# Kernel tuning notes

Measured on AMD Instinct MI355X. Metric: run time of the kernel, lower is better.

## Reference

```python
import jax, jax.numpy as jnp
import numpy as np
import math

SEQ = 2048
N_EMBD = 2048
N_HEAD = 16
DIM = N_EMBD // N_HEAD  # 128


def setup_inputs() -> dict:
    key = jax.random.key(0)
    k1, k2, k3, k4, k5 = jax.random.split(key, 5)
    s = 1.0 / math.sqrt(N_EMBD)
    return {
        "hidden_states": jax.random.normal(k1, (SEQ, N_EMBD), dtype=jnp.float32),
        "Wqkv": jax.random.normal(k2, (N_HEAD, N_EMBD, 3 * DIM), dtype=jnp.float32) * s,
        "bqkv": jax.random.normal(k3, (N_HEAD, 3 * DIM), dtype=jnp.float32) * 0.02,
        "Wout": jax.random.normal(k4, (N_EMBD, N_EMBD), dtype=jnp.float32) * s,
        "bout": jax.random.normal(k5, (N_EMBD,), dtype=jnp.float32) * 0.02,
    }


def reference(hidden_states, Wqkv, bqkv, Wout, bout):
    # per-head qkv projection: [h, s, 3*dim]
    qkv = jnp.einsum("se,hed->hsd", hidden_states, Wqkv) + bqkv[:, None, :]
    q, k, v = qkv[..., :DIM], qkv[..., DIM:2 * DIM], qkv[..., 2 * DIM:]
    # NOTE: original divides by sqrt(n_embd), not sqrt(head_dim)
    scale = 1.0 / math.sqrt(N_EMBD)
    scores = jnp.einsum("hsd,htd->hst", q, k) * scale  # [h, s, s]
    causal = jnp.tril(jnp.ones((SEQ, SEQ), dtype=bool))
    scores = jnp.where(causal[None], scores, -jnp.inf)
    probs = jax.nn.softmax(scores, axis=-1)
    out = jnp.einsum("hst,htd->hsd", probs, v)  # [h, s, dim]
    out = jnp.transpose(out, (1, 0, 2)).reshape(SEQ, N_EMBD)  # concat heads
    return out @ Wout + bout
```

## Files before the change

### kernel.cpp

```cpp
#include <hip/hip_runtime.h>
#include <cfloat>

#define SEQ   2048
#define NE    2048
#define NH    16
#define DIM   128
#define NKV   384
#define QSCALE 0.022097086912079611f

typedef __attribute__((ext_vector_type(8))) short bf16x8;
typedef __attribute__((ext_vector_type(4))) float f32x4;
typedef __attribute__((ext_vector_type(16))) float f32x16;
typedef __attribute__((ext_vector_type(8))) unsigned short u16x8;
typedef __attribute__((ext_vector_type(4))) unsigned int u32x4;
typedef __attribute__((ext_vector_type(2))) unsigned int u32x2;

#define PSLOT_B 16896u
#define NUNITS  768

__device__ __forceinline__ unsigned short f32_to_bf16_rn(float x) {
    unsigned u = __builtin_bit_cast(unsigned, x);
    u += 0x7fffu + ((u >> 16) & 1u);
    return (unsigned short)(u >> 16);
}

__device__ __forceinline__ unsigned cvt_pk_bf16(float lo, float hi) {
    unsigned r;
    asm("v_cvt_pk_bf16_f32 %0, %1, %2" : "=v"(r) : "v"(lo), "v"(hi));
    return r;
}
__device__ __forceinline__ float bf16lo(unsigned w) {
    return __builtin_bit_cast(float, w << 16);
}
__device__ __forceinline__ float bf16hi(unsigned w) {
    return __builtin_bit_cast(float, w & 0xFFFF0000u);
}

__device__ __forceinline__ void gload16(const void* g, void* l) {
    __builtin_amdgcn_global_load_lds(
        (const __attribute__((address_space(1))) unsigned int*)g,
        (__attribute__((address_space(3))) unsigned int*)l, 16, 0, 0);
}

__global__ __launch_bounds__(256) void convert_bf16_kernel(
    const float* __restrict__ src, unsigned short* __restrict__ dst, int n4)
{
    for (int i = blockIdx.x * 256 + threadIdx.x; i < n4; i += gridDim.x * 256) {
        float4 x = ((const float4*)src)[i];
        ushort4 h;
        h.x = f32_to_bf16_rn(x.x);
        h.y = f32_to_bf16_rn(x.y);
        h.z = f32_to_bf16_rn(x.z);
        h.w = f32_to_bf16_rn(x.w);
        ((ushort4*)dst)[i] = h;
    }
}

__global__ __launch_bounds__(256) void transpose_bf16_kernel(
    const float* __restrict__ src, unsigned short* __restrict__ dst, int K, int N)
{
    const int kt = blockIdx.x, nt = blockIdx.y, b = blockIdx.z;
    const float* s = src + (size_t)b * K * N;
    __shared__ float tile[64][65];
    const int tid = threadIdx.x;
    #pragma unroll
    for (int i = 0; i < 4; i++) {
        int idx = tid + 256 * i;
        int kk = idx >> 4, n4 = idx & 15;
        float4 val = *(const float4*)&s[(size_t)(kt * 64 + kk) * N + nt * 64 + n4 * 4];
        tile[kk][n4 * 4 + 0] = val.x; tile[kk][n4 * 4 + 1] = val.y;
        tile[kk][n4 * 4 + 2] = val.z; tile[kk][n4 * 4 + 3] = val.w;
    }
    __syncthreads();
    #pragma unroll
    for (int i = 0; i < 2; i++) {
        int idx = tid + 256 * i;
        int nn = idx >> 3, k8 = idx & 7;
        u16x8 hv;
        #pragma unroll
        for (int j = 0; j < 8; j++)
            hv[j] = f32_to_bf16_rn(tile[k8 * 8 + j][nn]);
        size_t off = ((size_t)b * N + nt * 64 + nn) * K + kt * 64 + k8 * 8;
        *(u16x8*)&dst[off] = hv;
    }
}

__global__ __launch_bounds__(256, 3) void gemm_qkv_kernel(
    const unsigned short* __restrict__ A, const unsigned short* __restrict__ B,
    const float* __restrict__ bias,
    unsigned short* __restrict__ o0, unsigned short* __restrict__ o1,
    unsigned short* __restrict__ o2)
{
    __shared__ unsigned short smem[2][128][64];
    const int tid = threadIdx.x;
    const int wave = tid >> 6, lane = tid & 63;
    const int s0 = blockIdx.x * 128, n0 = blockIdx.y * 128, z = blockIdx.z;
    const int bRowBase = z * NKV + n0;

    const int srow = lane >> 3;
    const int sswz = ((lane & 7) ^ srow) << 4;
    size_t aoff[4], boff[4];
    #pragma unroll
    for (int j = 0; j < 4; j++) {
        int ra = s0 + wave * 32 + j * 8 + srow;
        int rb = bRowBase + wave * 32 + j * 8 + srow;
        aoff[j] = 2 * ((size_t)ra * NE) + sswz;
        boff[j] = 2 * ((size_t)rb * NE) + sswz;
    }
    const char* pA = (const char*)A;
    const char* pB = (const char*)B;

    f32x4 acc[4][4];
    #pragma unroll
    for (int i = 0; i < 4; i++)
        #pragma unroll
        for (int j = 0; j < 4; j++) acc[i][j] = (f32x4){0.f, 0.f, 0.f, 0.f};

    const int wm = wave >> 1, wn = wave & 1;
    const int fr = lane & 15, kg = lane >> 4;

    for (int k0 = 0; k0 < NE; k0 += 64) {
        #pragma unroll
        for (int j = 0; j < 4; j++) {
            gload16(pA + aoff[j], &smem[0][wave * 32 + j * 8][0]);
            gload16(pB + boff[j], &smem[1][wave * 32 + j * 8][0]);
            aoff[j] += 128; boff[j] += 128;
        }
        __syncthreads();

        #pragma unroll
        for (int kh = 0; kh < 2; kh++) {
            bf16x8 af[4], bf[4];
            #pragma unroll
            for (int f = 0; f < 4; f++) {
                int ra = wm * 64 + f * 16 + fr;
                int ca = ((kh * 4 + kg) ^ (ra & 7)) << 4;
                af[f] = *(const bf16x8*)((const char*)&smem[0][0][0] + ra * 128 + ca);
                int rb = wn * 64 + f * 16 + fr;
                int cb = ((kh * 4 + kg) ^ (rb & 7)) << 4;
                bf[f] = *(const bf16x8*)((const char*)&smem[1][0][0] + rb * 128 + cb);
            }
            #pragma unroll
            for (int fm = 0; fm < 4; fm++)
                #pragma unroll
                for (int fn = 0; fn < 4; fn++)
                    acc[fm][fn] = __builtin_amdgcn_mfma_f32_16x16x32_bf16(
                        af[fm], bf[fn], acc[fm][fn], 0, 0, 0);
        }
        __syncthreads();
    }

    #pragma unroll
    for (int fm = 0; fm < 4; fm++)
        #pragma unroll
        for (int fn = 0; fn < 4; fn++) {
            int col = wn * 64 + fn * 16 + fr;
            int row = wm * 64 + fm * 16 + kg * 4;
            const int seg = n0 >> 7;
            unsigned short* dst = (seg == 0) ? o0 : ((seg == 1) ? o1 : o2);
            const float mult = (seg == 0) ? QSCALE : 1.f;
            float bv = bias[z * NKV + n0 + col];
            #pragma unroll
            for (int r = 0; r < 4; r++)
                dst[((size_t)(z * SEQ + s0 + row + r)) * DIM + col] =
                    f32_to_bf16_rn((acc[fm][fn][r] + bv) * mult);
        }
}

__global__ __launch_bounds__(128, 3) void gemm_out_kernel(
    const unsigned short* __restrict__ A, const unsigned short* __restrict__ B,
    const float* __restrict__ bias, float* __restrict__ out)
{
    __shared__ unsigned short As[64][64];
    __shared__ unsigned short Bs[128][64];
    const int tid = threadIdx.x;
    const int wave = tid >> 6, lane = tid & 63;
    const int s0 = blockIdx.x * 64, n0 = blockIdx.y * 128;

    const int srow = lane >> 3;
    const int sswz = ((lane & 7) ^ srow) << 4;
    size_t aoff[2], boff[4];
    #pragma unroll
    for (int j = 0; j < 2; j++) {
        int ra = s0 + wave * 32 + j * 16 + (srow + ((lane & 7) >= 0 ? 0 : 0));
        (void)ra;
    }
    size_t aof[4];
    #pragma unroll
    for (int j = 0; j < 4; j++) {
        int ra = s0 + wave * 32 + j * 8 + srow;
        aof[j] = 2 * ((size_t)ra * NE) + sswz;
    }
    #pragma unroll
    for (int j = 0; j < 4; j++) {
        int rb = n0 + wave * 64 + j * 8 + srow;
        boff[j] = 2 * ((size_t)rb * NE) + sswz;
    }
    size_t boff2[4];
    #pragma unroll
    for (int j = 0; j < 4; j++) {
        int rb = n0 + wave * 64 + 32 + j * 8 + srow;
        boff2[j] = 2 * ((size_t)rb * NE) + sswz;
    }
    const char* pA = (const char*)A;
    const char* pB = (const char*)B;

    f32x4 acc[4][4];
    #pragma unroll
    for (int i = 0; i < 4; i++)
        #pragma unroll
        for (int j = 0; j < 4; j++) acc[i][j] = (f32x4){0.f, 0.f, 0.f, 0.f};

    const int fr = lane & 15, kg = lane >> 4;

    for (int k0 = 0; k0 < NE; k0 += 64) {
        #pragma unroll
        for (int j = 0; j < 4; j++) {
            gload16(pA + aof[j], &As[wave * 32 + j * 8][0]);
            gload16(pB + boff[j], &Bs[wave * 64 + j * 8][0]);
            gload16(pB + boff2[j], &Bs[wave * 64 + 32 + j * 8][0]);
            aof[j] += 128; boff[j] += 128; boff2[j] += 128;
        }
        __syncthreads();

        #pragma unroll
        for (int kh = 0; kh < 2; kh++) {
            bf16x8 af[4], bf[4];
            #pragma unroll
            for (int f = 0; f < 4; f++) {
                int ra = f * 16 + fr;
                int ca = ((kh * 4 + kg) ^ (ra & 7)) << 4;
                af[f] = *(const bf16x8*)((const char*)&As[0][0] + ra * 128 + ca);
                int rb = wave * 64 + f * 16 + fr;
                int cb = ((kh * 4 + kg) ^ (rb & 7)) << 4;
                bf[f] = *(const bf16x8*)((const char*)&Bs[0][0] + rb * 128 + cb);
            }
            #pragma unroll
            for (int fm = 0; fm < 4; fm++)
                #pragma unroll
                for (int fn = 0; fn < 4; fn++)
                    acc[fm][fn] = __builtin_amdgcn_mfma_f32_16x16x32_bf16(
                        af[fm], bf[fn], acc[fm][fn], 0, 0, 0);
        }
        __syncthreads();
    }

    #pragma unroll
    for (int fm = 0; fm < 4; fm++)
        #pragma unroll
        for (int fn = 0; fn < 4; fn++) {
            int col = n0 + wave * 64 + fn * 16 + fr;
            int row = s0 + fm * 16 + kg * 4;
            float bv = bias[col];
            #pragma unroll
            for (int r = 0; r < 4; r++)
                out[(size_t)(row + r) * NE + col] = acc[fm][fn][r] + bv;
        }
}

__global__ __launch_bounds__(128, 2) void attn_partial_kernel(
    const unsigned short* __restrict__ Qb, const unsigned short* __restrict__ Kb,
    const unsigned short* __restrict__ Vb, char* __restrict__ partB,
    unsigned short* __restrict__ AOb)
{
    const int uid = (int)blockIdx.x;
    const int h = uid & 15;
    const int u = uid >> 4;
    int qt, t_begin, t_end, chunk;
    bool direct;
    if (u < 16) {
        qt = 16 + u; t_begin = 0; t_end = 16; chunk = 0; direct = false;
    } else {
        int p = (u - 16) >> 1;
        if (((u - 16) & 1) == 0) { qt = 15 - p; t_begin = 0; t_end = qt + 1; chunk = 0; direct = true; }
        else                     { qt = 31 - p; t_begin = 16; t_end = qt + 1; chunk = 1; direct = false; }
    }
    char* slotB = partB + (size_t)((h * 16 + (qt - 16)) * 2 + chunk) * PSLOT_B;

    const char* kh = (const char*)(Kb + (size_t)h * SEQ * DIM);
    const unsigned short* vh = Vb + (size_t)h * SEQ * DIM;

    __shared__ __align__(16) unsigned short Klds[2][64 * 128];
    __shared__ __align__(16) unsigned short Vt[128][72];

    const int tid = threadIdx.x;
    const int w = tid >> 6, lane = tid & 63;
    const int cc = lane & 31, hh = lane >> 5;
    const int Q0 = qt * 64 + w * 32;

    bf16x8 qf[8];
    {
        const unsigned short* qrow = Qb + ((size_t)h * SEQ + Q0 + cc) * DIM;
        #pragma unroll
        for (int st = 0; st < 8; st++)
            qf[st] = *(const bf16x8*)&qrow[st * 16 + hh * 8];
    }

    const int key0 = (tid & 31) * 2;
    const int dbase = (tid >> 5) * 32;

    f32x16 oacc[4];
    #pragma unroll
    for (int dt = 0; dt < 4; dt++)
        #pragma unroll
        for (int r = 0; r < 16; r++) oacc[dt][r] = 0.f;
    float m_run = -FLT_MAX, l_run = 0.f;

    u16x8 vrA[4], vrB[4];

    {
        const int tb0 = t_begin * 64;
        #pragma unroll
        for (int j = 0; j < 8; j++) {
            int row = w * 32 + j * 4 + (lane >> 4);
            gload16(kh + (size_t)(tb0 + row) * 256 + (((lane & 15) ^ (row & 7)) << 4),
                    &Klds[0][(w * 32 + j * 4) * 128]);
        }
        const u16x8* p0 = (const u16x8*)&vh[(size_t)(tb0 + key0) * DIM + dbase];
        const u16x8* p1 = (const u16x8*)&vh[(size_t)(tb0 + key0 + 1) * DIM + dbase];
        #pragma unroll
        for (int q8 = 0; q8 < 4; q8++) { vrA[q8] = p0[q8]; vrB[q8] = p1[q8]; }
        #pragma unroll
        for (int q8 = 0; q8 < 4; q8++)
            #pragma unroll
            for (int j = 0; j < 8; j++)
                *(unsigned*)&Vt[dbase + q8 * 8 + j][key0] =
                    (unsigned)(unsigned short)vrA[q8][j] |
                    ((unsigned)(unsigned short)vrB[q8][j] << 16);
        asm volatile("s_waitcnt vmcnt(0)" ::: "memory");
        __syncthreads();
    }

    for (int t = t_begin; t < t_end; t++) {
        const int buf = (t - t_begin) & 1;
        const int t0 = t * 64;
        const bool notlast = (t + 1 < t_end);

        if (notlast) {
            const int t1 = t0 + 64;
            #pragma unroll
            for (int j = 0; j < 8; j++) {
                int row = w * 32 + j * 4 + (lane >> 4);
                gload16(kh + (size_t)(t1 + row) * 256 + (((lane & 15) ^ (row & 7)) << 4),
                        &Klds[buf ^ 1][(w * 32 + j * 4) * 128]);
            }
            const u16x8* p0 = (const u16x8*)&vh[(size_t)(t1 + key0) * DIM + dbase];
            const u16x8* p1 = (const u16x8*)&vh[(size_t)(t1 + key0 + 1) * DIM + dbase];
            #pragma unroll
            for (int q8 = 0; q8 < 4; q8++) { vrA[q8] = p0[q8]; vrB[q8] = p1[q8]; }
        }

        f32x16 s0, s1;
        #pragma unroll
        for (int r = 0; r < 16; r++) { s0[r] = 0.f; s1[r] = 0.f; }
        __builtin_amdgcn_s_setprio(1);
        #pragma unroll
        for (int st = 0; st < 8; st++) {
            int r0 = cc, r1 = 32 + cc;
            bf16x8 kf0 = *(const bf16x8*)((const char*)&Klds[buf][0] +
                            r0 * 256 + (((2 * st + hh) ^ (r0 & 7)) << 4));
            bf16x8 kf1 = *(const bf16x8*)((const char*)&Klds[buf][0] +
                            r1 * 256 + (((2 * st + hh) ^ (r1 & 7)) << 4));
            s0 = __builtin_amdgcn_mfma_f32_32x32x16_bf16(kf0, qf[st], s0, 0, 0, 0);
            s1 = __builtin_amdgcn_mfma_f32_32x32x16_bf16(kf1, qf[st], s1, 0, 0, 0);
        }
        __builtin_amdgcn_s_setprio(0);

        if (t == qt) {
            const int q = Q0 + cc;
            #pragma unroll
            for (int r = 0; r < 16; r++) {
                int krow = (r & 3) + 8 * (r >> 2) + 4 * hh;
                s0[r] = (t0 + krow > q) ? -3.0e38f : s0[r];
                s1[r] = (t0 + 32 + krow > q) ? -3.0e38f : s1[r];
            }
        }

        float t4[4];
        #pragma unroll
        for (int j = 0; j < 4; j++) t4[j] = fmaxf(s0[j], s1[j]);
        #pragma unroll
        for (int r = 4; r < 16; r++) t4[r & 3] = fmaxf(t4[r & 3], fmaxf(s0[r], s1[r]));
        float mx = fmaxf(fmaxf(t4[0], t4[1]), fmaxf(t4[2], t4[3]));
        mx = fmaxf(mx, __shfl_xor(mx, 32));
        const bool nog = __all((int)(mx - m_run <= 8.f));
        float sc = 1.f;
        if (!nog) {
            float m_new = fmaxf(m_run, mx);
            sc = __expf(m_run - m_new);
            m_run = m_new;
        }

        float e4[4] = {0.f, 0.f, 0.f, 0.f};
        #pragma unroll
        for (int r = 0; r < 16; r++) {
            s0[r] = __expf(s0[r] - m_run);
            s1[r] = __expf(s1[r] - m_run);
            e4[r & 3] += s0[r] + s1[r];
        }
        float psum = (e4[0] + e4[1]) + (e4[2] + e4[3]);
        psum += __shfl_xor(psum, 32);
        l_run = l_run * sc + psum;
        if (!nog) {
            #pragma unroll
            for (int dt = 0; dt < 4; dt++)
                #pragma unroll
                for (int r = 0; r < 16; r++) oacc[dt][r] *= sc;
        }

        unsigned pd[16];
        #pragma unroll
        for (int uu = 0; uu < 8; uu++) {
            pd[uu]     = cvt_pk_bf16(s0[2 * uu], s0[2 * uu + 1]);
            pd[8 + uu] = cvt_pk_bf16(s1[2 * uu], s1[2 * uu + 1]);
        }

        __builtin_amdgcn_s_setprio(1);
        #pragma unroll
        for (int km = 0; km < 4; km++) {
            u32x2 sA = __builtin_amdgcn_permlane32_swap(pd[4 * km + 0], pd[4 * km + 2], false, false);
            u32x2 sB = __builtin_amdgcn_permlane32_swap(pd[4 * km + 1], pd[4 * km + 3], false, false);
            u32x4 pw; pw[0] = sA[0]; pw[1] = sB[0]; pw[2] = sA[1]; pw[3] = sB[1];
            bf16x8 pb = __builtin_bit_cast(bf16x8, pw);
            #pragma unroll
            for (int dt = 0; dt < 4; dt++) {
                bf16x8 vf = *(const bf16x8*)&Vt[dt * 32 + cc][km * 16 + hh * 8];
                oacc[dt] = __builtin_amdgcn_mfma_f32_32x32x16_bf16(vf, pb, oacc[dt], 0, 0, 0);
            }
        }
        __builtin_amdgcn_s_setprio(0);

        if (notlast) {
            __syncthreads();
            #pragma unroll
            for (int q8 = 0; q8 < 4; q8++)
                #pragma unroll
                for (int j = 0; j < 8; j++)
                    *(unsigned*)&Vt[dbase + q8 * 8 + j][key0] =
                        (unsigned)(unsigned short)vrA[q8][j] |
                        ((unsigned)(unsigned short)vrB[q8][j] << 16);
            asm volatile("s_waitcnt vmcnt(0)" ::: "memory");
            __syncthreads();
        }
    }

    const int prow = w * 32 + cc;
    const float inv = 1.f / l_run;
    if (direct) {
        unsigned short* aorow = AOb + (size_t)(Q0 + cc) * NE + h * DIM;
        #pragma unroll
        for (int dt = 0; dt < 4; dt++)
            #pragma unroll
            for (int m = 0; m < 4; m++) {
                unsigned lo = cvt_pk_bf16(oacc[dt][4 * m + 0] * inv, oacc[dt][4 * m + 1] * inv);
                unsigned hi = cvt_pk_bf16(oacc[dt][4 * m + 2] * inv, oacc[dt][4 * m + 3] * inv);
                u32x2 pk; pk[0] = lo; pk[1] = hi;
                *(u32x2*)&aorow[dt * 32 + 8 * m + 4 * hh] = pk;
            }
    } else {
        float* mf = (float*)slotB;
        float* lf = mf + 64;
        if (hh == 0) { mf[prow] = m_run; lf[prow] = l_run; }
        unsigned short* orow = (unsigned short*)(slotB + 512) + (size_t)prow * 128;
        #pragma unroll
        for (int dt = 0; dt < 4; dt++)
            #pragma unroll
            for (int m = 0; m < 4; m++) {
                unsigned lo = cvt_pk_bf16(oacc[dt][4 * m + 0] * inv, oacc[dt][4 * m + 1] * inv);
                unsigned hi = cvt_pk_bf16(oacc[dt][4 * m + 2] * inv, oacc[dt][4 * m + 3] * inv);
                u32x2 pk; pk[0] = lo; pk[1] = hi;
                *(u32x2*)&orow[dt * 32 + 8 * m + 4 * hh] = pk;
            }
    }
}

__global__ __launch_bounds__(128) void attn_merge_kernel(
    const char* __restrict__ partB, unsigned short* __restrict__ AOb)
{
    const int blk = (int)blockIdx.x;
    const int h = blk >> 4, qtm = blk & 15;
    const char* s0B = partB + (size_t)((h * 16 + qtm) * 2) * PSLOT_B;
    const char* s1B = s0B + PSLOT_B;
    const float* m0 = (const float*)s0B; const float* l0 = m0 + 64;
    const float* m1 = (const float*)s1B; const float* l1 = m1 + 64;
    const unsigned short* O0 = (const unsigned short*)(s0B + 512);
    const unsigned short* O1 = (const unsigned short*)(s1B + 512);

    const int tid = threadIdx.x;
    const int f4 = tid & 31;
    const int rg = tid >> 5;

    #pragma unroll 1
    for (int j = 0; j < 16; j++) {
        const int row = rg + 4 * j;
        float M = fmaxf(m0[row], m1[row]);
        float w0 = __expf(m0[row] - M) * l0[row];
        float w1 = __expf(m1[row] - M) * l1[row];
        float inv = 1.f / (w0 + w1);
        w0 *= inv; w1 *= inv;
        u32x2 a = *(const u32x2*)&O0[(size_t)row * 128 + f4 * 4];
        u32x2 b = *(const u32x2*)&O1[(size_t)row * 128 + f4 * 4];
        float r0 = w0 * bf16lo(a[0]) + w1 * bf16lo(b[0]);
        float r1 = w0 * bf16hi(a[0]) + w1 * bf16hi(b[0]);
        float r2 = w0 * bf16lo(a[1]) + w1 * bf16lo(b[1]);
        float r3 = w0 * bf16hi(a[1]) + w1 * bf16hi(b[1]);
        u32x2 pk; pk[0] = cvt_pk_bf16(r0, r1); pk[1] = cvt_pk_bf16(r2, r3);
        *(u32x2*)&AOb[(size_t)((16 + qtm) * 64 + row) * NE + h * DIM + f4 * 4] = pk;
    }
}

extern "C" void kernel_launch(void* const* d_in, const int* in_sizes, int n_in,
                              void* d_out, int out_size, void* d_ws, size_t ws_size,
                              hipStream_t stream) {
    const float* H    = (const float*)d_in[0];
    const float* Wqkv = (const float*)d_in[1];
    const float* bqkv = (const float*)d_in[2];
    const float* Wout = (const float*)d_in[3];
    const float* bout = (const float*)d_in[4];
    float* out = (float*)d_out;

    char* W8 = (char*)d_ws;
    const size_t MiB = 1ull << 20;
    unsigned short* qb  = (unsigned short*)(W8 + 0);
    unsigned short* kb  = (unsigned short*)(W8 + 8 * MiB);
    unsigned short* vb  = (unsigned short*)(W8 + 16 * MiB);
    unsigned short* Wob = (unsigned short*)(W8 + 24 * MiB);
    unsigned short* AOb = (unsigned short*)(W8 + 32 * MiB);
    char* part          = (char*)(W8 + 40 * MiB);
    unsigned short* Hb  = (unsigned short*)(W8 + 49 * MiB);
    unsigned short* Wqb = (unsigned short*)(W8 + 57 * MiB);

    convert_bf16_kernel<<<1024, 256, 0, stream>>>(H, Hb, SEQ * NE / 4);
    transpose_bf16_kernel<<<dim3(NE / 64, NKV / 64, NH), 256, 0, stream>>>(
        Wqkv, Wqb, NE, NKV);
    transpose_bf16_kernel<<<dim3(NE / 64, NE / 64, 1), 256, 0, stream>>>(
        Wout, Wob, NE, NE);
    gemm_qkv_kernel<<<dim3(SEQ / 128, NKV / 128, NH), 256, 0, stream>>>(
        Hb, Wqb, bqkv, qb, kb, vb);
    attn_partial_kernel<<<dim3(NUNITS), 128, 0, stream>>>(qb, kb, vb, part, AOb);
    attn_merge_kernel<<<dim3(256), 128, 0, stream>>>(part, AOb);
    gemm_out_kernel<<<dim3(SEQ / 64, NE / 128), 128, 0, stream>>>(
        AOb, Wob, bout, out);
}
```

Before: 168.3 us.

## Load K fragments directly from global into registers instead of through LDS

The attention kernel now reads K tiles straight from global memory into per-lane MFMA fragment registers (kf0/kf1 arrays) and prefetches the next tile right after the QK MFMAs. This removes the double-buffered K LDS array, the async global-to-LDS copies and the vmcnt waits. It frees LDS, which may allow more blocks per CU. In exchange each wave issues its own global loads, duplicated across waves, and uses 32 extra VGPRs, which may reduce occupancy. The gemm_out offset setup is also tidied, without changing behaviour.

```diff
diff --git a/kernel.cpp b/kernel.cpp
--- a/kernel.cpp
+++ b/kernel.cpp
@@ -179,28 +179,15 @@
 
     const int srow = lane >> 3;
     const int sswz = ((lane & 7) ^ srow) << 4;
-    size_t aoff[2], boff[4];
-    #pragma unroll
-    for (int j = 0; j < 2; j++) {
-        int ra = s0 + wave * 32 + j * 16 + (srow + ((lane & 7) >= 0 ? 0 : 0));
-        (void)ra;
-    }
-    size_t aof[4];
+    size_t aof[4], boff[4], boff2[4];
     #pragma unroll
     for (int j = 0; j < 4; j++) {
         int ra = s0 + wave * 32 + j * 8 + srow;
         aof[j] = 2 * ((size_t)ra * NE) + sswz;
-    }
-    #pragma unroll
-    for (int j = 0; j < 4; j++) {
         int rb = n0 + wave * 64 + j * 8 + srow;
         boff[j] = 2 * ((size_t)rb * NE) + sswz;
-    }
-    size_t boff2[4];
-    #pragma unroll
-    for (int j = 0; j < 4; j++) {
-        int rb = n0 + wave * 64 + 32 + j * 8 + srow;
-        boff2[j] = 2 * ((size_t)rb * NE) + sswz;
+        int rb2 = n0 + wave * 64 + 32 + j * 8 + srow;
+        boff2[j] = 2 * ((size_t)rb2 * NE) + sswz;
     }
     const char* pA = (const char*)A;
     const char* pB = (const char*)B;
@@ -277,10 +264,9 @@
     }
     char* slotB = partB + (size_t)((h * 16 + (qt - 16)) * 2 + chunk) * PSLOT_B;
 
-    const char* kh = (const char*)(Kb + (size_t)h * SEQ * DIM);
+    const unsigned short* khp = Kb + (size_t)h * SEQ * DIM;
     const unsigned short* vh = Vb + (size_t)h * SEQ * DIM;
 
-    __shared__ __align__(16) unsigned short Klds[2][64 * 128];
     __shared__ __align__(16) unsigned short Vt[128][72];
 
     const int tid = threadIdx.x;
@@ -307,14 +293,16 @@
     float m_run = -FLT_MAX, l_run = 0.f;
 
     u16x8 vrA[4], vrB[4];
+    bf16x8 kf0[8], kf1[8];
 
     {
         const int tb0 = t_begin * 64;
-        #pragma unroll
-        for (int j = 0; j < 8; j++) {
-            int row = w * 32 + j * 4 + (lane >> 4);
-            gload16(kh + (size_t)(tb0 + row) * 256 + (((lane & 15) ^ (row & 7)) << 4),
-                    &Klds[0][(w * 32 + j * 4) * 128]);
+        const unsigned short* kr0 = khp + (size_t)(tb0 + cc) * DIM + hh * 8;
+        const unsigned short* kr1 = khp + (size_t)(tb0 + 32 + cc) * DIM + hh * 8;
+        #pragma unroll
+        for (int st = 0; st < 8; st++) {
+            kf0[st] = *(const bf16x8*)&kr0[st * 16];
+            kf1[st] = *(const bf16x8*)&kr1[st * 16];
         }
         const u16x8* p0 = (const u16x8*)&vh[(size_t)(tb0 + key0) * DIM + dbase];
         const u16x8* p1 = (const u16x8*)&vh[(size_t)(tb0 + key0 + 1) * DIM + dbase];
@@ -327,23 +315,15 @@
                 *(unsigned*)&Vt[dbase + q8 * 8 + j][key0] =
                     (unsigned)(unsigned short)vrA[q8][j] |
                     ((unsigned)(unsigned short)vrB[q8][j] << 16);
-        asm volatile("s_waitcnt vmcnt(0)" ::: "memory");
         __syncthreads();
     }
 
     for (int t = t_begin; t < t_end; t++) {
-        const int buf = (t - t_begin) & 1;
         const int t0 = t * 64;
         const bool notlast = (t + 1 < t_end);
+        const int t1 = t0 + 64;
 
         if (notlast) {
-            const int t1 = t0 + 64;
-            #pragma unroll
-            for (int j = 0; j < 8; j++) {
-                int row = w * 32 + j * 4 + (lane >> 4);
-                gload16(kh + (size_t)(t1 + row) * 256 + (((lane & 15) ^ (row & 7)) << 4),
-                        &Klds[buf ^ 1][(w * 32 + j * 4) * 128]);
-            }
             const u16x8* p0 = (const u16x8*)&vh[(size_t)(t1 + key0) * DIM + dbase];
             const u16x8* p1 = (const u16x8*)&vh[(size_t)(t1 + key0 + 1) * DIM + dbase];
             #pragma unroll
@@ -356,15 +336,20 @@
         __builtin_amdgcn_s_setprio(1);
         #pragma unroll
         for (int st = 0; st < 8; st++) {
-            int r0 = cc, r1 = 32 + cc;
-            bf16x8 kf0 = *(const bf16x8*)((const char*)&Klds[buf][0] +
-                            r0 * 256 + (((2 * st + hh) ^ (r0 & 7)) << 4));
-            bf16x8 kf1 = *(const bf16x8*)((const char*)&Klds[buf][0] +
-                            r1 * 256 + (((2 * st + hh) ^ (r1 & 7)) << 4));
-            s0 = __builtin_amdgcn_mfma_f32_32x32x16_bf16(kf0, qf[st], s0, 0, 0, 0);
-            s1 = __builtin_amdgcn_mfma_f32_32x32x16_bf16(kf1, qf[st], s1, 0, 0, 0);
+            s0 = __builtin_amdgcn_mfma_f32_32x32x16_bf16(kf0[st], qf[st], s0, 0, 0, 0);
+            s1 = __builtin_amdgcn_mfma_f32_32x32x16_bf16(kf1[st], qf[st], s1, 0, 0, 0);
         }
         __builtin_amdgcn_s_setprio(0);
+
+        if (notlast) {
+            const unsigned short* kr0 = khp + (size_t)(t1 + cc) * DIM + hh * 8;
+            const unsigned short* kr1 = khp + (size_t)(t1 + 32 + cc) * DIM + hh * 8;
+            #pragma unroll
+            for (int st = 0; st < 8; st++) {
+                kf0[st] = *(const bf16x8*)&kr0[st * 16];
+                kf1[st] = *(const bf16x8*)&kr1[st * 16];
+            }
+        }
 
         if (t == qt) {
             const int q = Q0 + cc;
@@ -439,7 +424,6 @@
                     *(unsigned*)&Vt[dbase + q8 * 8 + j][key0] =
                         (unsigned)(unsigned short)vrA[q8][j] |
                         ((unsigned)(unsigned short)vrB[q8][j] << 16);
-            asm volatile("s_waitcnt vmcnt(0)" ::: "memory");
             __syncthreads();
         }
     }
```

Measured after the change: 182.2 us. 1.08x slower.

## Single-buffer K tile in attention and raise QKV GEMM occupancy bound

Applied to the files above, without the earlier changes.

The attention kernel's K tile goes from double-buffered to single-buffered LDS. The next K tile is now loaded only after the post-PV barrier, so K loads no longer overlap the QK and softmax compute, but LDS per block shrinks and more blocks can share a CU. The QKV GEMM's launch bounds minimum blocks per CU goes from 3 to 4, which may limit registers. The output GEMM offset setup is also cleaned up, with dead code removed.

```diff
diff --git a/kernel.cpp b/kernel.cpp
--- a/kernel.cpp
+++ b/kernel.cpp
@@ -85,7 +85,7 @@
     }
 }
 
-__global__ __launch_bounds__(256, 3) void gemm_qkv_kernel(
+__global__ __launch_bounds__(256, 4) void gemm_qkv_kernel(
     const unsigned short* __restrict__ A, const unsigned short* __restrict__ B,
     const float* __restrict__ bias,
     unsigned short* __restrict__ o0, unsigned short* __restrict__ o1,
@@ -179,28 +179,15 @@
 
     const int srow = lane >> 3;
     const int sswz = ((lane & 7) ^ srow) << 4;
-    size_t aoff[2], boff[4];
-    #pragma unroll
-    for (int j = 0; j < 2; j++) {
-        int ra = s0 + wave * 32 + j * 16 + (srow + ((lane & 7) >= 0 ? 0 : 0));
-        (void)ra;
-    }
-    size_t aof[4];
+    size_t aof[4], boff[4], boff2[4];
     #pragma unroll
     for (int j = 0; j < 4; j++) {
         int ra = s0 + wave * 32 + j * 8 + srow;
         aof[j] = 2 * ((size_t)ra * NE) + sswz;
-    }
-    #pragma unroll
-    for (int j = 0; j < 4; j++) {
         int rb = n0 + wave * 64 + j * 8 + srow;
         boff[j] = 2 * ((size_t)rb * NE) + sswz;
-    }
-    size_t boff2[4];
-    #pragma unroll
-    for (int j = 0; j < 4; j++) {
-        int rb = n0 + wave * 64 + 32 + j * 8 + srow;
-        boff2[j] = 2 * ((size_t)rb * NE) + sswz;
+        int rb2 = n0 + wave * 64 + 32 + j * 8 + srow;
+        boff2[j] = 2 * ((size_t)rb2 * NE) + sswz;
     }
     const char* pA = (const char*)A;
     const char* pB = (const char*)B;
@@ -280,7 +267,7 @@
     const char* kh = (const char*)(Kb + (size_t)h * SEQ * DIM);
     const unsigned short* vh = Vb + (size_t)h * SEQ * DIM;
 
-    __shared__ __align__(16) unsigned short Klds[2][64 * 128];
+    __shared__ __align__(16) unsigned short Klds[64 * 128];
     __shared__ __align__(16) unsigned short Vt[128][72];
 
     const int tid = threadIdx.x;
@@ -314,7 +301,7 @@
         for (int j = 0; j < 8; j++) {
             int row = w * 32 + j * 4 + (lane >> 4);
             gload16(kh + (size_t)(tb0 + row) * 256 + (((lane & 15) ^ (row & 7)) << 4),
-                    &Klds[0][(w * 32 + j * 4) * 128]);
+                    &Klds[(w * 32 + j * 4) * 128]);
         }
         const u16x8* p0 = (const u16x8*)&vh[(size_t)(tb0 + key0) * DIM + dbase];
         const u16x8* p1 = (const u16x8*)&vh[(size_t)(tb0 + key0 + 1) * DIM + dbase];
@@ -332,18 +319,11 @@
     }
 
     for (int t = t_begin; t < t_end; t++) {
-        const int buf = (t - t_begin) & 1;
         const int t0 = t * 64;
         const bool notlast = (t + 1 < t_end);
+        const int t1 = t0 + 64;
 
         if (notlast) {
-            const int t1 = t0 + 64;
-            #pragma unroll
-            for (int j = 0; j < 8; j++) {
-                int row = w * 32 + j * 4 + (lane >> 4);
-                gload16(kh + (size_t)(t1 + row) * 256 + (((lane & 15) ^ (row & 7)) << 4),
-                        &Klds[buf ^ 1][(w * 32 + j * 4) * 128]);
-            }
             const u16x8* p0 = (const u16x8*)&vh[(size_t)(t1 + key0) * DIM + dbase];
             const u16x8* p1 = (const u16x8*)&vh[(size_t)(t1 + key0 + 1) * DIM + dbase];
             #pragma unroll
@@ -357,9 +337,9 @@
         #pragma unroll
         for (int st = 0; st < 8; st++) {
             int r0 = cc, r1 = 32 + cc;
-            bf16x8 kf0 = *(const bf16x8*)((const char*)&Klds[buf][0] +
+            bf16x8 kf0 = *(const bf16x8*)((const char*)&Klds[0] +
                             r0 * 256 + (((2 * st + hh) ^ (r0 & 7)) << 4));
-            bf16x8 kf1 = *(const bf16x8*)((const char*)&Klds[buf][0] +
+            bf16x8 kf1 = *(const bf16x8*)((const char*)&Klds[0] +
                             r1 * 256 + (((2 * st + hh) ^ (r1 & 7)) << 4));
             s0 = __builtin_amdgcn_mfma_f32_32x32x16_bf16(kf0, qf[st], s0, 0, 0, 0);
             s1 = __builtin_amdgcn_mfma_f32_32x32x16_bf16(kf1, qf[st], s1, 0, 0, 0);
@@ -432,6 +412,12 @@
 
         if (notlast) {
             __syncthreads();
+            #pragma unroll
+            for (int j = 0; j < 8; j++) {
+                int row = w * 32 + j * 4 + (lane >> 4);
+                gload16(kh + (size_t)(t1 + row) * 256 + (((lane & 15) ^ (row & 7)) << 4),
+                        &Klds[(w * 32 + j * 4) * 128]);
+            }
             #pragma unroll
             for (int q8 = 0; q8 < 4; q8++)
                 #pragma unroll
```

Result: no change. 167.8 us (-0.3%).
